# Kernel optimization log

Measured on AMD Instinct MI355X. Metric: run time of the kernel, lower is better.

The kernel has to match this reference:

```python
import jax, jax.numpy as jnp
import numpy as np

B, IN, OUT, E, K = 8192, 512, 720, 16, 2
MOE_TEMP = 1.0


def setup_inputs() -> dict:
    key = jax.random.key(0)
    ks = jax.random.split(key, 5)
    s_in = 1.0 / np.sqrt(IN)
    return {
        "x": jax.random.normal(ks[0], (B, IN), dtype=jnp.float32),
        "Wg": jax.random.normal(ks[1], (IN, E), dtype=jnp.float32) * s_in,
        "bg": jax.random.normal(ks[2], (E,), dtype=jnp.float32) * 0.01,
        "We": jax.random.normal(ks[3], (E, IN, OUT), dtype=jnp.float32) * s_in,
        "be": jax.random.normal(ks[4], (E, OUT), dtype=jnp.float32) * 0.01,
    }


def reference(x, Wg, bg, We, be):
    # Gating (eval mode: no noise, divide by temperature)
    gate = (x @ Wg + bg) / MOE_TEMP                      # [B, E]
    topk_vals, topk_idx = jax.lax.top_k(gate, K)          # [B, K]
    gates = jax.nn.softmax(topk_vals, axis=1)             # [B, K]

    # Dense all-expert forward (as the original module computes)
    expert_out = jnp.einsum('bi,eio->beo', x, We) + be    # [B, E, OUT]
    sel = jnp.take_along_axis(expert_out, topk_idx[:, :, None], axis=1)  # [B, K, OUT]
    output = jnp.sum(gates[:, :, None] * sel, axis=1)     # [B, OUT]

    # Load-balancing loss
    probs = jax.nn.softmax(gate, axis=1)                  # [B, E]
    assign = jnp.argmax(gate, axis=1)                     # [B]
    D = jnp.zeros((E,), dtype=gate.dtype).at[assign].add(1.0) / x.shape[0]
    P = jnp.mean(probs, axis=0)
    lb_loss = jnp.sum(D * P) * E
    return output, lb_loss
```

## Files before the change

kernel.cpp:

```cpp
#include <hip/hip_runtime.h>
#include <hip/hip_bf16.h>


#define BATCH 8192
#define IND   512
#define OUTD  720
#define NEXP  16
#define CPAD  16

typedef __attribute__((ext_vector_type(8))) short short8;
typedef __attribute__((ext_vector_type(4))) float floatx4;

__device__ __forceinline__ unsigned short f2bf(float f) {
    union { float f; unsigned u; } v; v.f = f;
    unsigned r = v.u + 0x7FFFu + ((v.u >> 16) & 1u);
    return (unsigned short)(r >> 16);
}

__global__ __launch_bounds__(256) void gate_kernel4(
    const float* __restrict__ x, const float* __restrict__ Wg,
    const float* __restrict__ bg,
    int* __restrict__ counts, float* __restrict__ Psum, float* __restrict__ Dsum,
    float* __restrict__ gates, unsigned short* __restrict__ lists,
    unsigned short* __restrict__ xb)
{
    __shared__ float sx[16][512];
    __shared__ float sWg[16][516];
    __shared__ float sg[16][17];
    __shared__ float Ploc[16], Dloc[16];
    __shared__ int   cnt_loc[16], base_loc[16], off_loc[16];

    int tid = threadIdx.x;
    if (tid < 16) { Ploc[tid] = 0.f; Dloc[tid] = 0.f; cnt_loc[tid] = 0; off_loc[tid] = 0; }

    int rbase = blockIdx.x * 16;

    const float4* gx4 = (const float4*)(x + (size_t)rbase * IND);
    #pragma unroll
    for (int j = 0; j < 8; ++j) {
        int f = tid + j * 256;
        int r = f >> 7;
        int c = f & 127;
        *(float4*)&sx[r][c * 4] = gx4[f];
    }
    const float4* gw4 = (const float4*)Wg;
    #pragma unroll
    for (int j = 0; j < 8; ++j) {
        int f = tid + j * 256;
        float4 v = gw4[f];
        int i  = f >> 2;
        int e0 = (f & 3) * 4;
        sWg[e0 + 0][i] = v.x;
        sWg[e0 + 1][i] = v.y;
        sWg[e0 + 2][i] = v.z;
        sWg[e0 + 3][i] = v.w;
    }
    __syncthreads();

    int r = tid >> 4, e = tid & 15;
    const float4* xr = (const float4*)&sx[r][0];
    const float4* wr = (const float4*)&sWg[e][0];
    float acc = bg[e];
    #pragma unroll 8
    for (int i4 = 0; i4 < 128; ++i4) {
        float4 a = xr[i4], w = wr[i4];
        acc += a.x * w.x + a.y * w.y + a.z * w.z + a.w * w.w;
    }
    sg[r][e] = acc;

    #pragma unroll
    for (int j = 0; j < 4; ++j) {
        int c  = tid + j * 256;
        int rr = c >> 6;
        int q  = c & 63;
        const float* sp = &sx[rr][q * 8];
        short8 o;
        #pragma unroll
        for (int t = 0; t < 8; ++t) o[t] = (short)f2bf(sp[t]);
        *(short8*)&xb[(size_t)(rbase + rr) * IND + q * 8] = o;
    }
    __syncthreads();

    int i0 = 0, i1 = 0;
    if (tid < 16) {
        int row = rbase + tid;
        float v0 = -1e30f, v1 = -1e30f;
        float g[16];
        #pragma unroll
        for (int ee = 0; ee < 16; ++ee) {
            float v = sg[tid][ee]; g[ee] = v;
            if (v > v0)      { v1 = v0; i1 = i0; v0 = v; i0 = ee; }
            else if (v > v1) { v1 = v;  i1 = ee; }
        }
        float e1   = expf(v1 - v0);
        float inv2 = 1.f / (1.f + e1);
        gates[row * 2 + 0] = inv2;
        gates[row * 2 + 1] = e1 * inv2;

        float s = 0.f, pr[16];
        #pragma unroll
        for (int ee = 0; ee < 16; ++ee) { pr[ee] = expf(g[ee] - v0); s += pr[ee]; }
        float invs = 1.f / s;
        #pragma unroll
        for (int ee = 0; ee < 16; ++ee) atomicAdd(&Ploc[ee], pr[ee] * invs);
        atomicAdd(&Dloc[i0], 1.f);
        atomicAdd(&cnt_loc[i0], 1);
        atomicAdd(&cnt_loc[i1], 1);
    }
    __syncthreads();

    if (tid < 16) {
        if (cnt_loc[tid] > 0) base_loc[tid] = atomicAdd(&counts[tid * CPAD], cnt_loc[tid]);
        atomicAdd(&Psum[tid * CPAD], Ploc[tid]);
        atomicAdd(&Dsum[tid * CPAD], Dloc[tid]);
    }
    __syncthreads();

    if (tid < 16) {
        int row = rbase + tid;
        int p0 = base_loc[i0] + atomicAdd(&off_loc[i0], 1);
        lists[i0 * BATCH + p0] = (unsigned short)(row << 1);
        int p1 = base_loc[i1] + atomicAdd(&off_loc[i1], 1);
        lists[i1 * BATCH + p1] = (unsigned short)((row << 1) | 1);
    }
}

__global__ __launch_bounds__(256) void transpose_We_kernel(
    const float* __restrict__ We, unsigned short* __restrict__ Wt)
{
    __shared__ float tile[32][69];
    int e  = blockIdx.z;
    int ob = blockIdx.x * 32;
    int kb = blockIdx.y * 64;
    int tid = threadIdx.x;
    const float* src = We + (size_t)e * (IND * OUTD);

    #pragma unroll
    for (int p = 0; p < 2; ++p) {
        int f  = tid + p * 256;
        int kk = f >> 3;
        int o4 = f & 7;
        float4 v = make_float4(0.f, 0.f, 0.f, 0.f);
        if (ob + o4 * 4 < OUTD)
            v = *(const float4*)&src[(size_t)(kb + kk) * OUTD + ob + o4 * 4];
        tile[o4 * 4 + 0][kk] = v.x;
        tile[o4 * 4 + 1][kk] = v.y;
        tile[o4 * 4 + 2][kk] = v.z;
        tile[o4 * 4 + 3][kk] = v.w;
    }
    __syncthreads();

    int o  = tid >> 3;
    int k8 = tid & 7;
    if (ob + o < OUTD) {
        const float* sp = &tile[o][k8 * 8];
        short8 w;
        #pragma unroll
        for (int t = 0; t < 8; ++t) w[t] = (short)f2bf(sp[t]);
        *(short8*)&Wt[(size_t)e * (OUTD * IND) + (size_t)(ob + o) * IND + kb + k8 * 8] = w;
    }
}

__global__ __launch_bounds__(256, 4) void moe_mfma_kernel(
    const unsigned short* __restrict__ xb, const unsigned short* __restrict__ Wt,
    const float* __restrict__ be,
    const int* __restrict__ counts, const float* __restrict__ gates,
    const unsigned short* __restrict__ lists,
    float* __restrict__ partial, float* __restrict__ out, int use_partial)
{
    int e = blockIdx.z;
    int n = counts[e * CPAD];
    int r0 = blockIdx.y * 128;
    if (r0 >= n) return;
    int n0 = blockIdx.x * 64;

    __shared__ unsigned short sA[128][72];
    __shared__ unsigned short sB[64][72];
    __shared__ int   srow[128];
    __shared__ float sgw[128];
    __shared__ unsigned short sent[128];

    int tid = threadIdx.x;
    if (tid < 128) {
        int idx = r0 + tid;
        if (idx < n) {
            int ent = lists[e * BATCH + idx];
            srow[tid] = ent >> 1;
            sgw[tid]  = gates[(ent >> 1) * 2 + (ent & 1)];
            sent[tid] = (unsigned short)ent;
        } else { srow[tid] = 0; sgw[tid] = 0.f; sent[tid] = 0; }
    }
    __syncthreads();

    int rA = tid >> 3, q8 = (tid & 7) * 8;
    const unsigned short* aptr[4];
    #pragma unroll
    for (int j = 0; j < 4; ++j)
        aptr[j] = xb + (size_t)srow[rA + j * 32] * IND + q8;
    const unsigned short* bptr[2];
    #pragma unroll
    for (int j = 0; j < 2; ++j) {
        int col = n0 + rA + j * 32;
        if (col >= OUTD) col = 0;
        bptr[j] = Wt + ((size_t)e * OUTD + col) * IND + q8;
    }

    int lane = tid & 63, wave = tid >> 6;
    int wm = (wave & 1) * 64, wn = (wave >> 1) * 32;
    int l15 = lane & 15, quad = lane >> 4;

    floatx4 acc[4][2] = {};

    for (int kt = 0; kt < IND / 64; ++kt) {
        short8 av[4], bv[2];
        #pragma unroll
        for (int j = 0; j < 4; ++j) av[j] = *(const short8*)(aptr[j] + kt * 64);
        #pragma unroll
        for (int j = 0; j < 2; ++j) bv[j] = *(const short8*)(bptr[j] + kt * 64);
        __syncthreads();
        #pragma unroll
        for (int j = 0; j < 4; ++j) *(short8*)&sA[rA + j * 32][q8] = av[j];
        #pragma unroll
        for (int j = 0; j < 2; ++j) *(short8*)&sB[rA + j * 32][q8] = bv[j];
        __syncthreads();
        #pragma unroll
        for (int ks = 0; ks < 2; ++ks) {
            int ko = ks * 32 + quad * 8;
            short8 a[4], b[2];
            #pragma unroll
            for (int i = 0; i < 4; ++i) a[i] = *(const short8*)&sA[wm + i * 16 + l15][ko];
            #pragma unroll
            for (int j = 0; j < 2; ++j) b[j] = *(const short8*)&sB[wn + j * 16 + l15][ko];
            #pragma unroll
            for (int i = 0; i < 4; ++i)
                #pragma unroll
                for (int j = 0; j < 2; ++j)
                    acc[i][j] = __builtin_amdgcn_mfma_f32_16x16x32_bf16(a[i], b[j], acc[i][j], 0, 0, 0);
        }
    }

    #pragma unroll
    for (int j = 0; j < 2; ++j) {
        int col = n0 + wn + j * 16 + l15;
        if (col < OUTD) {
            float bev = be[e * OUTD + col];
            #pragma unroll
            for (int i = 0; i < 4; ++i) {
                #pragma unroll
                for (int rr = 0; rr < 4; ++rr) {
                    int lm = wm + i * 16 + quad * 4 + rr;
                    if (r0 + lm < n) {
                        float val = sgw[lm] * (acc[i][j][rr] + bev);
                        if (use_partial)
                            partial[(size_t)sent[lm] * OUTD + col] = val;
                        else
                            atomicAdd(&out[(size_t)srow[lm] * OUTD + col], val);
                    }
                }
            }
        }
    }
}

__global__ __launch_bounds__(256) void combine_kernel(
    const float* __restrict__ partial, const float* __restrict__ Psum,
    const float* __restrict__ Dsum, float* __restrict__ out)
{
    unsigned f = blockIdx.x * 256 + threadIdx.x;
    unsigned b = f / 180u;
    unsigned o4 = (f - b * 180u) * 4u;
    const float* p0 = partial + (size_t)(2u * b) * OUTD + o4;
    float4 v0 = *(const float4*)p0;
    float4 v1 = *(const float4*)(p0 + OUTD);
    float4 rv;
    rv.x = v0.x + v1.x; rv.y = v0.y + v1.y; rv.z = v0.z + v1.z; rv.w = v0.w + v1.w;
    *(float4*)(out + (size_t)b * OUTD + o4) = rv;

    if (f == 0) {
        float s = 0.f;
        #pragma unroll
        for (int e = 0; e < NEXP; ++e)
            s += (Dsum[e * CPAD] / (float)BATCH) * (Psum[e * CPAD] / (float)BATCH);
        out[(size_t)BATCH * OUTD] = s * (float)NEXP;
    }
}

__global__ void loss_kernel(const float* __restrict__ Psum,
                            const float* __restrict__ Dsum,
                            float* __restrict__ out)
{
    if (threadIdx.x == 0) {
        float s = 0.f;
        #pragma unroll
        for (int e = 0; e < NEXP; ++e)
            s += (Dsum[e * CPAD] / (float)BATCH) * (Psum[e * CPAD] / (float)BATCH);
        out[(size_t)BATCH * OUTD] = s * (float)NEXP;
    }
}

extern "C" void kernel_launch(void* const* d_in, const int* in_sizes, int n_in,
                              void* d_out, int out_size, void* d_ws, size_t ws_size,
                              hipStream_t stream)
{
    const float* x  = (const float*)d_in[0];
    const float* Wg = (const float*)d_in[1];
    const float* bg = (const float*)d_in[2];
    const float* We = (const float*)d_in[3];
    const float* be = (const float*)d_in[4];
    float* out = (float*)d_out;

    char* ws = (char*)d_ws;
    int*   counts = (int*)ws;
    float* Psum   = (float*)(ws + 1024);
    float* Dsum   = (float*)(ws + 2048);
    float* gates  = (float*)(ws + 4096);
    unsigned short* lists = (unsigned short*)(ws + 4096 + BATCH * 2 * sizeof(float));
    size_t off_xb = 4096 + (size_t)BATCH * 2 * 4 + (size_t)NEXP * BATCH * 2;
    off_xb = (off_xb + 255) & ~(size_t)255;
    unsigned short* xb = (unsigned short*)(ws + off_xb);
    size_t off_wt = off_xb + (size_t)BATCH * IND * 2;
    unsigned short* Wt = (unsigned short*)(ws + off_wt);
    size_t off_pt = off_wt + (size_t)NEXP * OUTD * IND * 2;
    float* partial = (float*)(ws + off_pt);
    size_t req = off_pt + (size_t)BATCH * 2 * OUTD * sizeof(float);

    int use_partial = (ws_size >= req) ? 1 : 0;

    hipMemsetAsync(ws, 0, 4096, stream);
    if (!use_partial)
        hipMemsetAsync(d_out, 0, (size_t)out_size * sizeof(float), stream);

    gate_kernel4<<<BATCH / 16, 256, 0, stream>>>(x, Wg, bg, counts, Psum, Dsum, gates, lists, xb);

    dim3 tgrid((OUTD + 31) / 32, IND / 64, NEXP);
    transpose_We_kernel<<<tgrid, 256, 0, stream>>>(We, Wt);

    dim3 grid((OUTD + 63) / 64, BATCH / 128, NEXP);
    moe_mfma_kernel<<<grid, 256, 0, stream>>>(xb, Wt, be, counts, gates, lists,
                                              partial, out, use_partial);

    if (use_partial) {
        combine_kernel<<<(BATCH * (OUTD / 4)) / 256, 256, 0, stream>>>(partial, Psum, Dsum, out);
    } else {
        loss_kernel<<<1, 64, 0, stream>>>(Psum, Dsum, out);
    }
}
```

Measured before the change: 174.7 us.

## Fuse gate and weight transpose, use direct-to-LDS loads with swizzle, bf16 partials

Gate computation and expert weight transpose/bf16 conversion are merged into one launch, with block ranges split by role. The grouped GEMM widens its N tile to 96 and loads A/B tiles with global_load_lds into an XOR-swizzled, unpadded LDS layout. Intermediate partial outputs are stored as bf16 to halve their traffic, and the atomic fallback path is dropped. The unified 67KB shared buffer lowers occupancy of the gate blocks, and bf16 partials reduce output precision.

```diff
diff --git a/kernel.cpp b/kernel.cpp
--- a/kernel.cpp
+++ b/kernel.cpp
@@ -16,148 +16,162 @@
     unsigned r = v.u + 0x7FFFu + ((v.u >> 16) & 1u);
     return (unsigned short)(r >> 16);
 }
-
-__global__ __launch_bounds__(256) void gate_kernel4(
+__device__ __forceinline__ float bf2f(unsigned short u) {
+    union { unsigned u; float f; } v; v.u = ((unsigned)u) << 16;
+    return v.f;
+}
+
+__device__ __forceinline__ void gl2lds16(const void* g, void* l) {
+    __builtin_amdgcn_global_load_lds(
+        (const __attribute__((address_space(1))) void*)g,
+        (__attribute__((address_space(3))) void*)l, 16, 0, 0);
+}
+
+__global__ __launch_bounds__(256) void prep_kernel(
     const float* __restrict__ x, const float* __restrict__ Wg,
-    const float* __restrict__ bg,
+    const float* __restrict__ bg, const float* __restrict__ We,
     int* __restrict__ counts, float* __restrict__ Psum, float* __restrict__ Dsum,
     float* __restrict__ gates, unsigned short* __restrict__ lists,
-    unsigned short* __restrict__ xb)
+    unsigned short* __restrict__ xb, unsigned short* __restrict__ Wt)
 {
-    __shared__ float sx[16][512];
-    __shared__ float sWg[16][516];
-    __shared__ float sg[16][17];
-    __shared__ float Ploc[16], Dloc[16];
-    __shared__ int   cnt_loc[16], base_loc[16], off_loc[16];
-
+    __shared__ __align__(16) char smem[67328];
     int tid = threadIdx.x;
-    if (tid < 16) { Ploc[tid] = 0.f; Dloc[tid] = 0.f; cnt_loc[tid] = 0; off_loc[tid] = 0; }
-
-    int rbase = blockIdx.x * 16;
-
-    const float4* gx4 = (const float4*)(x + (size_t)rbase * IND);
-    #pragma unroll
-    for (int j = 0; j < 8; ++j) {
-        int f = tid + j * 256;
-        int r = f >> 7;
-        int c = f & 127;
-        *(float4*)&sx[r][c * 4] = gx4[f];
-    }
-    const float4* gw4 = (const float4*)Wg;
-    #pragma unroll
-    for (int j = 0; j < 8; ++j) {
-        int f = tid + j * 256;
-        float4 v = gw4[f];
-        int i  = f >> 2;
-        int e0 = (f & 3) * 4;
-        sWg[e0 + 0][i] = v.x;
-        sWg[e0 + 1][i] = v.y;
-        sWg[e0 + 2][i] = v.z;
-        sWg[e0 + 3][i] = v.w;
-    }
-    __syncthreads();
-
-    int r = tid >> 4, e = tid & 15;
-    const float4* xr = (const float4*)&sx[r][0];
-    const float4* wr = (const float4*)&sWg[e][0];
-    float acc = bg[e];
-    #pragma unroll 8
-    for (int i4 = 0; i4 < 128; ++i4) {
-        float4 a = xr[i4], w = wr[i4];
-        acc += a.x * w.x + a.y * w.y + a.z * w.z + a.w * w.w;
-    }
-    sg[r][e] = acc;
-
-    #pragma unroll
-    for (int j = 0; j < 4; ++j) {
-        int c  = tid + j * 256;
-        int rr = c >> 6;
-        int q  = c & 63;
-        const float* sp = &sx[rr][q * 8];
-        short8 o;
-        #pragma unroll
-        for (int t = 0; t < 8; ++t) o[t] = (short)f2bf(sp[t]);
-        *(short8*)&xb[(size_t)(rbase + rr) * IND + q * 8] = o;
-    }
-    __syncthreads();
-
-    int i0 = 0, i1 = 0;
-    if (tid < 16) {
-        int row = rbase + tid;
-        float v0 = -1e30f, v1 = -1e30f;
-        float g[16];
-        #pragma unroll
-        for (int ee = 0; ee < 16; ++ee) {
-            float v = sg[tid][ee]; g[ee] = v;
-            if (v > v0)      { v1 = v0; i1 = i0; v0 = v; i0 = ee; }
-            else if (v > v1) { v1 = v;  i1 = ee; }
-        }
-        float e1   = expf(v1 - v0);
-        float inv2 = 1.f / (1.f + e1);
-        gates[row * 2 + 0] = inv2;
-        gates[row * 2 + 1] = e1 * inv2;
-
-        float s = 0.f, pr[16];
-        #pragma unroll
-        for (int ee = 0; ee < 16; ++ee) { pr[ee] = expf(g[ee] - v0); s += pr[ee]; }
-        float invs = 1.f / s;
-        #pragma unroll
-        for (int ee = 0; ee < 16; ++ee) atomicAdd(&Ploc[ee], pr[ee] * invs);
-        atomicAdd(&Dloc[i0], 1.f);
-        atomicAdd(&cnt_loc[i0], 1);
-        atomicAdd(&cnt_loc[i1], 1);
-    }
-    __syncthreads();
-
-    if (tid < 16) {
-        if (cnt_loc[tid] > 0) base_loc[tid] = atomicAdd(&counts[tid * CPAD], cnt_loc[tid]);
-        atomicAdd(&Psum[tid * CPAD], Ploc[tid]);
-        atomicAdd(&Dsum[tid * CPAD], Dloc[tid]);
-    }
-    __syncthreads();
-
-    if (tid < 16) {
-        int row = rbase + tid;
-        int p0 = base_loc[i0] + atomicAdd(&off_loc[i0], 1);
-        lists[i0 * BATCH + p0] = (unsigned short)(row << 1);
-        int p1 = base_loc[i1] + atomicAdd(&off_loc[i1], 1);
-        lists[i1 * BATCH + p1] = (unsigned short)((row << 1) | 1);
-    }
-}
-
-__global__ __launch_bounds__(256) void transpose_We_kernel(
-    const float* __restrict__ We, unsigned short* __restrict__ Wt)
-{
-    __shared__ float tile[32][69];
-    int e  = blockIdx.z;
-    int ob = blockIdx.x * 32;
-    int kb = blockIdx.y * 64;
-    int tid = threadIdx.x;
-    const float* src = We + (size_t)e * (IND * OUTD);
-
-    #pragma unroll
-    for (int p = 0; p < 2; ++p) {
-        int f  = tid + p * 256;
-        int kk = f >> 3;
-        int o4 = f & 7;
-        float4 v = make_float4(0.f, 0.f, 0.f, 0.f);
-        if (ob + o4 * 4 < OUTD)
-            v = *(const float4*)&src[(size_t)(kb + kk) * OUTD + ob + o4 * 4];
-        tile[o4 * 4 + 0][kk] = v.x;
-        tile[o4 * 4 + 1][kk] = v.y;
-        tile[o4 * 4 + 2][kk] = v.z;
-        tile[o4 * 4 + 3][kk] = v.w;
-    }
-    __syncthreads();
-
-    int o  = tid >> 3;
-    int k8 = tid & 7;
-    if (ob + o < OUTD) {
-        const float* sp = &tile[o][k8 * 8];
-        short8 w;
-        #pragma unroll
-        for (int t = 0; t < 8; ++t) w[t] = (short)f2bf(sp[t]);
-        *(short8*)&Wt[(size_t)e * (OUTD * IND) + (size_t)(ob + o) * IND + kb + k8 * 8] = w;
+
+    if (blockIdx.x < 512) {
+        float* sx   = (float*)smem;
+        float* sWg  = sx + 16 * 512;
+        float* sg   = sWg + 16 * 516;
+        float* Ploc = sg + 16 * 17;
+        float* Dloc = Ploc + 16;
+        int* cnt_loc  = (int*)(Dloc + 16);
+        int* base_loc = cnt_loc + 16;
+        int* off_loc  = base_loc + 16;
+
+        if (tid < 16) { Ploc[tid] = 0.f; Dloc[tid] = 0.f; cnt_loc[tid] = 0; off_loc[tid] = 0; }
+
+        int rbase = blockIdx.x * 16;
+
+        const float4* gx4 = (const float4*)(x + (size_t)rbase * IND);
+        #pragma unroll
+        for (int j = 0; j < 8; ++j) {
+            int f = tid + j * 256;
+            int r = f >> 7;
+            int c = f & 127;
+            *(float4*)&sx[r * 512 + c * 4] = gx4[f];
+        }
+        const float4* gw4 = (const float4*)Wg;
+        #pragma unroll
+        for (int j = 0; j < 8; ++j) {
+            int f = tid + j * 256;
+            float4 v = gw4[f];
+            int i  = f >> 2;
+            int e0 = (f & 3) * 4;
+            sWg[(e0 + 0) * 516 + i] = v.x;
+            sWg[(e0 + 1) * 516 + i] = v.y;
+            sWg[(e0 + 2) * 516 + i] = v.z;
+            sWg[(e0 + 3) * 516 + i] = v.w;
+        }
+        __syncthreads();
+
+        int r = tid >> 4, e = tid & 15;
+        const float4* xr = (const float4*)&sx[r * 512];
+        const float4* wr = (const float4*)&sWg[e * 516];
+        float acc = bg[e];
+        #pragma unroll 8
+        for (int i4 = 0; i4 < 128; ++i4) {
+            float4 a = xr[i4], w = wr[i4];
+            acc += a.x * w.x + a.y * w.y + a.z * w.z + a.w * w.w;
+        }
+        sg[r * 17 + e] = acc;
+
+        #pragma unroll
+        for (int j = 0; j < 4; ++j) {
+            int c  = tid + j * 256;
+            int rr = c >> 6;
+            int q  = c & 63;
+            const float* sp = &sx[rr * 512 + q * 8];
+            short8 o;
+            #pragma unroll
+            for (int t = 0; t < 8; ++t) o[t] = (short)f2bf(sp[t]);
+            *(short8*)&xb[(size_t)(rbase + rr) * IND + q * 8] = o;
+        }
+        __syncthreads();
+
+        int i0 = 0, i1 = 0;
+        if (tid < 16) {
+            int row = rbase + tid;
+            float v0 = -1e30f, v1 = -1e30f;
+            float g[16];
+            #pragma unroll
+            for (int ee = 0; ee < 16; ++ee) {
+                float v = sg[tid * 17 + ee]; g[ee] = v;
+                if (v > v0)      { v1 = v0; i1 = i0; v0 = v; i0 = ee; }
+                else if (v > v1) { v1 = v;  i1 = ee; }
+            }
+            float e1   = expf(v1 - v0);
+            float inv2 = 1.f / (1.f + e1);
+            gates[row * 2 + 0] = inv2;
+            gates[row * 2 + 1] = e1 * inv2;
+
+            float s = 0.f, pr[16];
+            #pragma unroll
+            for (int ee = 0; ee < 16; ++ee) { pr[ee] = expf(g[ee] - v0); s += pr[ee]; }
+            float invs = 1.f / s;
+            #pragma unroll
+            for (int ee = 0; ee < 16; ++ee) atomicAdd(&Ploc[ee], pr[ee] * invs);
+            atomicAdd(&Dloc[i0], 1.f);
+            atomicAdd(&cnt_loc[i0], 1);
+            atomicAdd(&cnt_loc[i1], 1);
+        }
+        __syncthreads();
+
+        if (tid < 16) {
+            if (cnt_loc[tid] > 0) base_loc[tid] = atomicAdd(&counts[tid * CPAD], cnt_loc[tid]);
+            atomicAdd(&Psum[tid * CPAD], Ploc[tid]);
+            atomicAdd(&Dsum[tid * CPAD], Dloc[tid]);
+        }
+        __syncthreads();
+
+        if (tid < 16) {
+            int row = rbase + tid;
+            int p0 = base_loc[i0] + atomicAdd(&off_loc[i0], 1);
+            lists[i0 * BATCH + p0] = (unsigned short)(row << 1);
+            int p1 = base_loc[i1] + atomicAdd(&off_loc[i1], 1);
+            lists[i1 * BATCH + p1] = (unsigned short)((row << 1) | 1);
+        }
+    } else {
+        float* tile = (float*)smem;
+        int t  = blockIdx.x - 512;
+        int e  = t / 184;
+        int rem = t - e * 184;
+        int kb = (rem / 23) * 64;
+        int ob = (rem % 23) * 32;
+        const float* src = We + (size_t)e * (IND * OUTD);
+
+        #pragma unroll
+        for (int p = 0; p < 2; ++p) {
+            int f  = tid + p * 256;
+            int kk = f >> 3;
+            int o4 = f & 7;
+            float4 v = make_float4(0.f, 0.f, 0.f, 0.f);
+            if (ob + o4 * 4 < OUTD)
+                v = *(const float4*)&src[(size_t)(kb + kk) * OUTD + ob + o4 * 4];
+            tile[(o4 * 4 + 0) * 69 + kk] = v.x;
+            tile[(o4 * 4 + 1) * 69 + kk] = v.y;
+            tile[(o4 * 4 + 2) * 69 + kk] = v.z;
+            tile[(o4 * 4 + 3) * 69 + kk] = v.w;
+        }
+        __syncthreads();
+
+        int o  = tid >> 3;
+        int k8 = tid & 7;
+        if (ob + o < OUTD) {
+            const float* sp = &tile[o * 69 + k8 * 8];
+            short8 w;
+            #pragma unroll
+            for (int q = 0; q < 8; ++q) w[q] = (short)f2bf(sp[q]);
+            *(short8*)&Wt[(size_t)e * (OUTD * IND) + (size_t)(ob + o) * IND + kb + k8 * 8] = w;
+        }
     }
 }
 
@@ -166,16 +180,16 @@
     const float* __restrict__ be,
     const int* __restrict__ counts, const float* __restrict__ gates,
     const unsigned short* __restrict__ lists,
-    float* __restrict__ partial, float* __restrict__ out, int use_partial)
+    unsigned short* __restrict__ partial)
 {
     int e = blockIdx.z;
     int n = counts[e * CPAD];
     int r0 = blockIdx.y * 128;
     if (r0 >= n) return;
-    int n0 = blockIdx.x * 64;
-
-    __shared__ unsigned short sA[128][72];
-    __shared__ unsigned short sB[64][72];
+    int n0 = blockIdx.x * 96;
+
+    __shared__ unsigned short sA[128][64];
+    __shared__ unsigned short sB[96][64];
     __shared__ int   srow[128];
     __shared__ float sgw[128];
     __shared__ unsigned short sent[128];
@@ -192,55 +206,60 @@
     }
     __syncthreads();
 
-    int rA = tid >> 3, q8 = (tid & 7) * 8;
-    const unsigned short* aptr[4];
+    int lane = tid & 63, wave = tid >> 6;
+    int lsub = lane >> 3;
+    int swz  = (lane & 7) ^ lsub;
+
+    const unsigned short* aglb[4];
+    unsigned short* alds[4];
     #pragma unroll
-    for (int j = 0; j < 4; ++j)
-        aptr[j] = xb + (size_t)srow[rA + j * 32] * IND + q8;
-    const unsigned short* bptr[2];
+    for (int g = 0; g < 4; ++g) {
+        int row = wave * 32 + g * 8 + lsub;
+        aglb[g] = xb + (size_t)srow[row] * IND + swz * 8;
+        alds[g] = &sA[wave * 32 + g * 8][0];
+    }
+    const unsigned short* bglb[3];
+    unsigned short* blds[3];
     #pragma unroll
-    for (int j = 0; j < 2; ++j) {
-        int col = n0 + rA + j * 32;
+    for (int g = 0; g < 3; ++g) {
+        int col = n0 + wave * 24 + g * 8 + lsub;
         if (col >= OUTD) col = 0;
-        bptr[j] = Wt + ((size_t)e * OUTD + col) * IND + q8;
-    }
-
-    int lane = tid & 63, wave = tid >> 6;
-    int wm = (wave & 1) * 64, wn = (wave >> 1) * 32;
+        bglb[g] = Wt + ((size_t)e * OUTD + col) * IND + swz * 8;
+        blds[g] = &sB[wave * 24 + g * 8][0];
+    }
+
     int l15 = lane & 15, quad = lane >> 4;
-
-    floatx4 acc[4][2] = {};
+    int wm = (wave & 1) * 64, wn = (wave >> 1) * 48;
+    int axor = (l15 & 7) * 8;
+
+    floatx4 acc[4][3] = {};
 
     for (int kt = 0; kt < IND / 64; ++kt) {
-        short8 av[4], bv[2];
-        #pragma unroll
-        for (int j = 0; j < 4; ++j) av[j] = *(const short8*)(aptr[j] + kt * 64);
-        #pragma unroll
-        for (int j = 0; j < 2; ++j) bv[j] = *(const short8*)(bptr[j] + kt * 64);
-        __syncthreads();
-        #pragma unroll
-        for (int j = 0; j < 4; ++j) *(short8*)&sA[rA + j * 32][q8] = av[j];
-        #pragma unroll
-        for (int j = 0; j < 2; ++j) *(short8*)&sB[rA + j * 32][q8] = bv[j];
-        __syncthreads();
+        __syncthreads();
+        #pragma unroll
+        for (int g = 0; g < 4; ++g) gl2lds16(aglb[g] + kt * 64, alds[g]);
+        #pragma unroll
+        for (int g = 0; g < 3; ++g) gl2lds16(bglb[g] + kt * 64, blds[g]);
+        __syncthreads();
+
         #pragma unroll
         for (int ks = 0; ks < 2; ++ks) {
-            int ko = ks * 32 + quad * 8;
-            short8 a[4], b[2];
+            int ko = ((ks * 4 + quad) * 8) ^ axor;
+            short8 a[4], b[3];
             #pragma unroll
             for (int i = 0; i < 4; ++i) a[i] = *(const short8*)&sA[wm + i * 16 + l15][ko];
             #pragma unroll
-            for (int j = 0; j < 2; ++j) b[j] = *(const short8*)&sB[wn + j * 16 + l15][ko];
+            for (int j = 0; j < 3; ++j) b[j] = *(const short8*)&sB[wn + j * 16 + l15][ko];
             #pragma unroll
             for (int i = 0; i < 4; ++i)
                 #pragma unroll
-                for (int j = 0; j < 2; ++j)
+                for (int j = 0; j < 3; ++j)
                     acc[i][j] = __builtin_amdgcn_mfma_f32_16x16x32_bf16(a[i], b[j], acc[i][j], 0, 0, 0);
         }
     }
 
     #pragma unroll
-    for (int j = 0; j < 2; ++j) {
+    for (int j = 0; j < 3; ++j) {
         int col = n0 + wn + j * 16 + l15;
         if (col < OUTD) {
             float bev = be[e * OUTD + col];
@@ -251,10 +270,7 @@
                     int lm = wm + i * 16 + quad * 4 + rr;
                     if (r0 + lm < n) {
                         float val = sgw[lm] * (acc[i][j][rr] + bev);
-                        if (use_partial)
-                            partial[(size_t)sent[lm] * OUTD + col] = val;
-                        else
-                            atomicAdd(&out[(size_t)srow[lm] * OUTD + col], val);
+                        partial[(size_t)sent[lm] * OUTD + col] = f2bf(val);
                     }
                 }
             }
@@ -263,33 +279,23 @@
 }
 
 __global__ __launch_bounds__(256) void combine_kernel(
-    const float* __restrict__ partial, const float* __restrict__ Psum,
+    const unsigned short* __restrict__ partial, const float* __restrict__ Psum,
     const float* __restrict__ Dsum, float* __restrict__ out)
 {
     unsigned f = blockIdx.x * 256 + threadIdx.x;
     unsigned b = f / 180u;
     unsigned o4 = (f - b * 180u) * 4u;
-    const float* p0 = partial + (size_t)(2u * b) * OUTD + o4;
-    float4 v0 = *(const float4*)p0;
-    float4 v1 = *(const float4*)(p0 + OUTD);
+    const unsigned short* p0 = partial + (size_t)(2u * b) * OUTD + o4;
+    ushort4 u0 = *(const ushort4*)p0;
+    ushort4 u1 = *(const ushort4*)(p0 + OUTD);
     float4 rv;
-    rv.x = v0.x + v1.x; rv.y = v0.y + v1.y; rv.z = v0.z + v1.z; rv.w = v0.w + v1.w;
+    rv.x = bf2f(u0.x) + bf2f(u1.x);
+    rv.y = bf2f(u0.y) + bf2f(u1.y);
+    rv.z = bf2f(u0.z) + bf2f(u1.z);
+    rv.w = bf2f(u0.w) + bf2f(u1.w);
     *(float4*)(out + (size_t)b * OUTD + o4) = rv;
 
     if (f == 0) {
-        float s = 0.f;
-        #pragma unroll
-        for (int e = 0; e < NEXP; ++e)
-            s += (Dsum[e * CPAD] / (float)BATCH) * (Psum[e * CPAD] / (float)BATCH);
-        out[(size_t)BATCH * OUTD] = s * (float)NEXP;
-    }
-}
-
-__global__ void loss_kernel(const float* __restrict__ Psum,
-                            const float* __restrict__ Dsum,
-                            float* __restrict__ out)
-{
-    if (threadIdx.x == 0) {
         float s = 0.f;
         #pragma unroll
         for (int e = 0; e < NEXP; ++e)
@@ -321,27 +327,15 @@
     size_t off_wt = off_xb + (size_t)BATCH * IND * 2;
     unsigned short* Wt = (unsigned short*)(ws + off_wt);
     size_t off_pt = off_wt + (size_t)NEXP * OUTD * IND * 2;
-    float* partial = (float*)(ws + off_pt);
-    size_t req = off_pt + (size_t)BATCH * 2 * OUTD * sizeof(float);
-
-    int use_partial = (ws_size >= req) ? 1 : 0;
+    unsigned short* partial = (unsigned short*)(ws + off_pt);
 
     hipMemsetAsync(ws, 0, 4096, stream);
-    if (!use_partial)
-        hipMemsetAsync(d_out, 0, (size_t)out_size * sizeof(float), stream);
-
-    gate_kernel4<<<BATCH / 16, 256, 0, stream>>>(x, Wg, bg, counts, Psum, Dsum, gates, lists, xb);
-
-    dim3 tgrid((OUTD + 31) / 32, IND / 64, NEXP);
-    transpose_We_kernel<<<tgrid, 256, 0, stream>>>(We, Wt);
-
-    dim3 grid((OUTD + 63) / 64, BATCH / 128, NEXP);
-    moe_mfma_kernel<<<grid, 256, 0, stream>>>(xb, Wt, be, counts, gates, lists,
-                                              partial, out, use_partial);
-
-    if (use_partial) {
-        combine_kernel<<<(BATCH * (OUTD / 4)) / 256, 256, 0, stream>>>(partial, Psum, Dsum, out);
-    } else {
-        loss_kernel<<<1, 64, 0, stream>>>(Psum, Dsum, out);
-    }
-}
+
+    prep_kernel<<<512 + 2944, 256, 0, stream>>>(x, Wg, bg, We, counts, Psum, Dsum,
+                                                gates, lists, xb, Wt);
+
+    dim3 grid(8, 16, NEXP);
+    moe_mfma_kernel<<<grid, 256, 0, stream>>>(xb, Wt, be, counts, gates, lists, partial);
+
+    combine_kernel<<<(BATCH * (OUTD / 4)) / 256, 256, 0, stream>>>(partial, Psum, Dsum, out);
+}
```

After: 170.3 us. -2.5%, faster.
